# Kernel optimization log

Measured on AMD Instinct MI355X. Metric: run time of the kernel, lower is better.

Reference implementation:

```python
import jax, jax.numpy as jnp
import numpy as np

HEADS = 8
IN_CH = 768
INNER = 768
DK = INNER // HEADS


def setup_inputs() -> dict:
    key = jax.random.key(0)
    ks = jax.random.split(key, 9)
    bs, hw = 16, 1024
    s = 1.0 / np.sqrt(IN_CH)
    sp = 1.0 / np.sqrt(INNER)
    return {
        "x": jax.random.normal(ks[0], (bs, hw, IN_CH), jnp.float32),
        # weights stored (in, out) so y = x @ W + b (equiv to torch Linear)
        "Wq": jax.random.uniform(ks[1], (IN_CH, INNER), jnp.float32, -s, s),
        "bq": jax.random.uniform(ks[2], (INNER,), jnp.float32, -s, s),
        "Wk": jax.random.uniform(ks[3], (IN_CH, INNER), jnp.float32, -s, s),
        "bk": jax.random.uniform(ks[4], (INNER,), jnp.float32, -s, s),
        "Wv": jax.random.uniform(ks[5], (IN_CH, INNER), jnp.float32, -s, s),
        "bv": jax.random.uniform(ks[6], (INNER,), jnp.float32, -s, s),
        "Wp": jax.random.uniform(ks[7], (INNER, IN_CH), jnp.float32, -sp, sp),
        "bp": jax.random.uniform(ks[8], (IN_CH,), jnp.float32, -sp, sp),
    }


def reference(x, Wq, bq, Wk, bk, Wv, bv, Wp, bp):
    bs, hw, _ = x.shape
    # NOTE: the original torch code does .view(bs, heads, hw, dk) on a
    # (bs, hw, inner) tensor — a raw row-major reshape, not a head-split
    # transpose. Replicate exactly.
    q = (x @ Wq + bq).reshape(bs, HEADS, hw, DK)
    k = (x @ Wk + bk).reshape(bs, HEADS, hw, DK)
    v = (x @ Wv + bv).reshape(bs, HEADS, hw, DK)
    logits = jnp.einsum("bhqd,bhkd->bhqk", q, k) / np.sqrt(DK).astype(np.float32)
    attn = jax.nn.softmax(logits, axis=-1)
    out = jnp.einsum("bhqk,bhkd->bhqd", attn, v).reshape(bs, hw, INNER)
    # dropout is identity in eval mode
    return out @ Wp + bp
```

## Files before the change

kernel.cpp:

```cpp
#include <hip/hip_runtime.h>
#include <math.h>

typedef __bf16 bf16;
typedef __attribute__((ext_vector_type(8))) __bf16 bf16x8;
typedef __attribute__((ext_vector_type(4))) __bf16 bf16x4;
typedef __attribute__((ext_vector_type(4))) float f32x4;
typedef __attribute__((ext_vector_type(16))) float f32x16;

#define CE 0.14724445f
#define THR_RAW 54.0f

#define GLOAD16(g, l)                                                          \
    __builtin_amdgcn_global_load_lds(                                          \
        (const __attribute__((address_space(1))) void*)(g),                    \
        (__attribute__((address_space(3))) void*)(l), 16, 0, 0)

__global__ __launch_bounds__(256) void cvt_x(const float* __restrict__ x, bf16* __restrict__ xb) {
    size_t i = ((size_t)blockIdx.x * 256 + threadIdx.x) * 4;
    f32x4 v = *(const f32x4*)(x + i);
    bf16x4 o;
    o[0] = (bf16)v[0]; o[1] = (bf16)v[1]; o[2] = (bf16)v[2]; o[3] = (bf16)v[3];
    *(bf16x4*)(xb + i) = o;
}

struct WArgs { const float* w[4]; };

__global__ __launch_bounds__(256) void transpose_w(WArgs wa, bf16* __restrict__ out) {
    __shared__ float t[32][33];
    const int z = blockIdx.z;
    const float* __restrict__ W = wa.w[z];
    bf16* __restrict__ Wt = out + (size_t)z * 589824;
    int k0 = blockIdx.x * 32, n0 = blockIdx.y * 32;
    int tx = threadIdx.x, ty = threadIdx.y;
#pragma unroll
    for (int j = 0; j < 4; ++j)
        t[ty + j * 8][tx] = W[(size_t)(k0 + ty + j * 8) * 768 + n0 + tx];
    __syncthreads();
#pragma unroll
    for (int j = 0; j < 4; ++j)
        Wt[(size_t)(n0 + ty + j * 8) * 768 + k0 + tx] = (bf16)t[tx][ty + j * 8];
}

struct GemmArgs {
    const bf16* Bt[3];
    const float* bias[3];
    void* out[3];
};

template <bool F32OUT, int NZ>
__global__ __launch_bounds__(256, 2) void gemm_kernel(const bf16* __restrict__ A, GemmArgs ga) {
    __shared__ __align__(16) bf16 As[128 * 64];
    __shared__ __align__(16) bf16 Bs[128 * 64];
    const int nwg = gridDim.x;
    const int bid = blockIdx.x;
    const int lid = (bid & 7) * (nwg >> 3) + (bid >> 3);
    const int mt = lid / (6 * NZ);
    const int r0 = lid - mt * (6 * NZ);
    const int z  = r0 / 6;
    const int nt = r0 - z * 6;
    const int m0 = mt * 128;
    const int n0 = nt * 128;
    const bf16* __restrict__ Bt = ga.Bt[z];
    const int tid = threadIdx.x;
    const int lane = tid & 63, l15 = lane & 15, lq = lane >> 4;
    const int wid = tid >> 6;
    const int wm = (wid >> 1) * 64, wn = (wid & 1) * 64;

    const bf16* asrc[4]; const bf16* bsrc[4]; bf16* adst[4]; bf16* bdst[4];
#pragma unroll
    for (int i = 0; i < 4; ++i) {
        int r = (wid * 4 + i) * 8 + (lane >> 3);
        int s = lane & 7;
        int c = s ^ (r & 7);
        asrc[i] = A + (size_t)(m0 + r) * 768 + c * 8;
        bsrc[i] = Bt + (size_t)(n0 + r) * 768 + c * 8;
        adst[i] = As + (wid * 4 + i) * 512;
        bdst[i] = Bs + (wid * 4 + i) * 512;
    }

    f32x4 acc[4][4] = {};

    for (int ks = 0; ks < 768; ks += 64) {
#pragma unroll
        for (int i = 0; i < 4; ++i) {
            GLOAD16(asrc[i] + ks, adst[i]);
            GLOAD16(bsrc[i] + ks, bdst[i]);
        }
        __syncthreads();
#pragma unroll
        for (int kk = 0; kk < 2; ++kk) {
            bf16x8 af[4], bfr[4];
#pragma unroll
            for (int f = 0; f < 4; ++f) {
                int ar = wm + f * 16 + l15;
                int ac = (kk * 4 + lq) ^ (ar & 7);
                af[f] = *(const bf16x8*)(As + ar * 64 + ac * 8);
                int br = wn + f * 16 + l15;
                int bc = (kk * 4 + lq) ^ (br & 7);
                bfr[f] = *(const bf16x8*)(Bs + br * 64 + bc * 8);
            }
#pragma unroll
            for (int mf = 0; mf < 4; ++mf)
#pragma unroll
                for (int nf = 0; nf < 4; ++nf)
                    acc[mf][nf] = __builtin_amdgcn_mfma_f32_16x16x32_bf16(af[mf], bfr[nf], acc[mf][nf], 0, 0, 0);
        }
        __syncthreads();
    }
    const float* __restrict__ bias = ga.bias[z];
#pragma unroll
    for (int nf = 0; nf < 4; ++nf) {
        int col = n0 + wn + nf * 16 + l15;
        float bv = bias[col];
#pragma unroll
        for (int mf = 0; mf < 4; ++mf) {
            int rbase = m0 + wm + mf * 16 + lq * 4;
#pragma unroll
            for (int i = 0; i < 4; ++i) {
                float v = acc[mf][nf][i] + bv;
                if constexpr (F32OUT)
                    ((float*)ga.out[z])[(size_t)(rbase + i) * 768 + col] = v;
                else
                    ((bf16*)ga.out[z])[(size_t)(rbase + i) * 768 + col] = (bf16)v;
            }
        }
    }
}

__global__ __launch_bounds__(256) void transpose_v(const bf16* __restrict__ V, bf16* __restrict__ Vt) {
    __shared__ unsigned short t[64 * 97];
    const int g = blockIdx.y;
    const int kv0 = blockIdx.x * 64;
    const unsigned short* __restrict__ Vg = (const unsigned short*)V + (size_t)g * 98304;
    unsigned short* __restrict__ Vtg = (unsigned short*)Vt + (size_t)g * 98304;
    const int tid = threadIdx.x;
#pragma unroll
    for (int p = 0; p < 24; ++p) {
        int id = tid + p * 256;
        int row = id / 96, col = id % 96;
        t[row * 97 + col] = Vg[(size_t)(kv0 + row) * 96 + col];
    }
    __syncthreads();
#pragma unroll
    for (int p = 0; p < 24; ++p) {
        int id = tid + p * 256;
        int d = id >> 6, j = id & 63;
        Vtg[(size_t)d * 1024 + kv0 + j] = t[j * 97 + d];
    }
}

static __device__ inline int pk2(float a, float b) {
    union { __bf16 h[2]; int w; } u;
    u.h[0] = (__bf16)a; u.h[1] = (__bf16)b;
    return u.w;
}

static __device__ inline bf16x8 pack_step(float p0, float p1, float p2, float p3,
                                          float p4, float p5, float p6, float p7, int hi) {
    int A0 = pk2(p0, p1), A1 = pk2(p2, p3);
    int B0 = pk2(p4, p5), B1 = pk2(p6, p7);
    int t0 = hi ? A0 : B0;
    int t1 = hi ? A1 : B1;
    int x0 = __shfl_xor(t0, 32);
    int x1 = __shfl_xor(t1, 32);
    union { int w[4]; bf16x8 v; } u;
    u.w[0] = hi ? x0 : A0;
    u.w[1] = hi ? x1 : A1;
    u.w[2] = hi ? B0 : x0;
    u.w[3] = hi ? B1 : x1;
    return u.v;
}

__global__ __launch_bounds__(256, 3) void attn_kernel(const bf16* __restrict__ Q, const bf16* __restrict__ K,
                                                      const bf16* __restrict__ Vt, bf16* __restrict__ AO) {
    __shared__ __align__(16) bf16 Ks[12 * 64 * 8];
    __shared__ __align__(16) bf16 Vss[2 * 8 * 96 * 8];
    const int g = blockIdx.x;
    const int q0 = blockIdx.y * 128;
    const int tid = threadIdx.x;
    const int lane = tid & 63;
    const int l31 = lane & 31, hi = lane >> 5, wid = tid >> 6;
    const int qrow = q0 + wid * 32 + l31;
    const size_t gbase = (size_t)g * 98304;
    const bf16* __restrict__ Qg = Q + gbase;
    const bf16* __restrict__ Kg = K + gbase;
    const bf16* __restrict__ Vg = Vt + gbase;
    bf16* __restrict__ Og = AO + gbase;

    const bf16* ksrc[3]; bf16* kdst[3];
#pragma unroll
    for (int i = 0; i < 3; ++i) {
        int slot = wid * 3 + i;
        ksrc[i] = Kg + (size_t)lane * 96 + slot * 8;
        kdst[i] = Ks + slot * 512;
    }
    const bf16* vsrc[3]; int vdoff[3];
#pragma unroll
    for (int i = 0; i < 3; ++i) {
        int f = (wid * 3 + i) * 64 + lane;
        int slot = f / 96, row = f - slot * 96;
        vsrc[i] = Vg + (size_t)row * 1024 + slot * 8;
        vdoff[i] = (wid * 3 + i) * 512;
    }

    bf16x8 qf[6];
#pragma unroll
    for (int kk = 0; kk < 6; ++kk)
        qf[kk] = *(const bf16x8*)(Qg + (size_t)qrow * 96 + kk * 16 + hi * 8);

#pragma unroll
    for (int i = 0; i < 3; ++i) GLOAD16(ksrc[i], kdst[i]);
#pragma unroll
    for (int i = 0; i < 3; ++i) GLOAD16(vsrc[i], Vss + vdoff[i]);
    __syncthreads();
#pragma unroll
    for (int i = 0; i < 3; ++i) GLOAD16(vsrc[i] + 64, Vss + 6144 + vdoff[i]);

    f32x16 o[3] = {};
    float mrun = -INFINITY, lrun = 0.f;

    const bf16* kbase = Ks + hi * 512 + l31 * 8;

    for (int kt = 0; kt < 16; ++kt) {
        const bf16* vbase = Vss + (kt & 1) * 6144 + hi * 768 + l31 * 8;

        f32x16 s0 = {}, s1 = {};
        __builtin_amdgcn_s_setprio(1);
#pragma unroll
        for (int kk = 0; kk < 6; ++kk) {
            bf16x8 k0 = *(const bf16x8*)(kbase + kk * 1024);
            bf16x8 k1 = *(const bf16x8*)(kbase + kk * 1024 + 256);
            s0 = __builtin_amdgcn_mfma_f32_32x32x16_bf16(k0, qf[kk], s0, 0, 0, 0);
            s1 = __builtin_amdgcn_mfma_f32_32x32x16_bf16(k1, qf[kk], s1, 0, 0, 0);
        }
        __builtin_amdgcn_s_setprio(0);
        __syncthreads();
        if (kt < 15) {
#pragma unroll
            for (int i = 0; i < 3; ++i) GLOAD16(ksrc[i] + (kt + 1) * 6144, kdst[i]);
        }

        float t0 = fmaxf(fmaxf(s0[0], s0[1]), fmaxf(s0[2], s0[3]));
        float t1 = fmaxf(fmaxf(s0[4], s0[5]), fmaxf(s0[6], s0[7]));
        float t2 = fmaxf(fmaxf(s0[8], s0[9]), fmaxf(s0[10], s0[11]));
        float t3 = fmaxf(fmaxf(s0[12], s0[13]), fmaxf(s0[14], s0[15]));
        float u0 = fmaxf(fmaxf(s1[0], s1[1]), fmaxf(s1[2], s1[3]));
        float u1 = fmaxf(fmaxf(s1[4], s1[5]), fmaxf(s1[6], s1[7]));
        float u2 = fmaxf(fmaxf(s1[8], s1[9]), fmaxf(s1[10], s1[11]));
        float u3 = fmaxf(fmaxf(s1[12], s1[13]), fmaxf(s1[14], s1[15]));
        float pmax = fmaxf(fmaxf(fmaxf(t0, t1), fmaxf(t2, t3)),
                           fmaxf(fmaxf(u0, u1), fmaxf(u2, u3)));
        pmax = fmaxf(pmax, __shfl_xor(pmax, 32));
        if (!__all(pmax - mrun <= THR_RAW)) {
            float newm = fmaxf(mrun, pmax);
            float alpha = __builtin_amdgcn_exp2f(CE * (mrun - newm));
            mrun = newm;
            lrun *= alpha;
#pragma unroll
            for (int df = 0; df < 3; ++df)
#pragma unroll
                for (int r = 0; r < 16; ++r) o[df][r] *= alpha;
        }
        float lsa = 0.f, lsb = 0.f;
#pragma unroll
        for (int r = 0; r < 16; ++r) {
            float p = __builtin_amdgcn_exp2f(CE * (s0[r] - mrun));
            s0[r] = p; lsa += p;
        }
#pragma unroll
        for (int r = 0; r < 16; ++r) {
            float p = __builtin_amdgcn_exp2f(CE * (s1[r] - mrun));
            s1[r] = p; lsb += p;
        }
        float lsum = lsa + lsb;
        lsum += __shfl_xor(lsum, 32);
        lrun += lsum;

        bf16x8 pb0 = pack_step(s0[0], s0[1], s0[2], s0[3], s0[4], s0[5], s0[6], s0[7], hi);
        bf16x8 pb1 = pack_step(s0[8], s0[9], s0[10], s0[11], s0[12], s0[13], s0[14], s0[15], hi);
        bf16x8 pb2 = pack_step(s1[0], s1[1], s1[2], s1[3], s1[4], s1[5], s1[6], s1[7], hi);
        bf16x8 pb3 = pack_step(s1[8], s1[9], s1[10], s1[11], s1[12], s1[13], s1[14], s1[15], hi);
        __builtin_amdgcn_s_setprio(1);
#pragma unroll
        for (int df = 0; df < 3; ++df) {
            bf16x8 v0 = *(const bf16x8*)(vbase + 0 * 1536 + df * 256);
            bf16x8 v1 = *(const bf16x8*)(vbase + 1 * 1536 + df * 256);
            bf16x8 v2 = *(const bf16x8*)(vbase + 2 * 1536 + df * 256);
            bf16x8 v3 = *(const bf16x8*)(vbase + 3 * 1536 + df * 256);
            o[df] = __builtin_amdgcn_mfma_f32_32x32x16_bf16(v0, pb0, o[df], 0, 0, 0);
            o[df] = __builtin_amdgcn_mfma_f32_32x32x16_bf16(v1, pb1, o[df], 0, 0, 0);
            o[df] = __builtin_amdgcn_mfma_f32_32x32x16_bf16(v2, pb2, o[df], 0, 0, 0);
            o[df] = __builtin_amdgcn_mfma_f32_32x32x16_bf16(v3, pb3, o[df], 0, 0, 0);
        }
        __builtin_amdgcn_s_setprio(0);
        __syncthreads();
        if (kt < 14) {
#pragma unroll
            for (int i = 0; i < 3; ++i)
                GLOAD16(vsrc[i] + (kt + 2) * 64, Vss + (kt & 1) * 6144 + vdoff[i]);
        }
    }

    float inv = 1.0f / lrun;
#pragma unroll
    for (int df = 0; df < 3; ++df)
#pragma unroll
        for (int rq = 0; rq < 4; ++rq) {
            bf16x4 ov;
#pragma unroll
            for (int j = 0; j < 4; ++j) ov[j] = (bf16)(o[df][rq * 4 + j] * inv);
            *(bf16x4*)(Og + (size_t)qrow * 96 + df * 32 + rq * 8 + hi * 4) = ov;
        }
}

extern "C" void kernel_launch(void* const* d_in, const int* in_sizes, int n_in,
                              void* d_out, int out_size, void* d_ws, size_t ws_size,
                              hipStream_t stream) {
    const float* x  = (const float*)d_in[0];
    const float* Wq = (const float*)d_in[1];
    const float* bq = (const float*)d_in[2];
    const float* Wk = (const float*)d_in[3];
    const float* bk = (const float*)d_in[4];
    const float* Wv = (const float*)d_in[5];
    const float* bv = (const float*)d_in[6];
    const float* Wp = (const float*)d_in[7];
    const float* bp = (const float*)d_in[8];

    char* ws = (char*)d_ws;
    bf16* xb  = (bf16*)(ws);
    bf16* wt  = (bf16*)(ws + 25165824);
    bf16* Qb  = (bf16*)(ws + 29884416);
    bf16* Kb  = (bf16*)(ws + 55050240);
    bf16* Vb  = (bf16*)(ws + 80216064);
    bf16* Vtb = (bf16*)(ws + 105381888);
    bf16* AO  = xb;

    cvt_x<<<12288, 256, 0, stream>>>(x, xb);

    WArgs wa;
    wa.w[0] = Wq; wa.w[1] = Wk; wa.w[2] = Wv; wa.w[3] = Wp;
    transpose_w<<<dim3(24, 24, 4), dim3(32, 8), 0, stream>>>(wa, wt);

    GemmArgs g1{};
    g1.Bt[0] = wt;            g1.Bt[1] = wt + 589824;  g1.Bt[2] = wt + 2 * 589824;
    g1.bias[0] = bq;          g1.bias[1] = bk;         g1.bias[2] = bv;
    g1.out[0] = Qb;           g1.out[1] = Kb;          g1.out[2] = Vb;
    gemm_kernel<false, 3><<<2304, 256, 0, stream>>>(xb, g1);

    transpose_v<<<dim3(16, 128), 256, 0, stream>>>(Vb, Vtb);

    attn_kernel<<<dim3(128, 8), 256, 0, stream>>>(Qb, Kb, Vtb, AO);

    GemmArgs g2{};
    g2.Bt[0] = wt + 3 * 589824; g2.bias[0] = bp; g2.out[0] = (void*)d_out;
    g2.Bt[1] = g2.Bt[0]; g2.Bt[2] = g2.Bt[0];
    g2.bias[1] = bp; g2.bias[2] = bp;
    g2.out[1] = g2.out[0]; g2.out[2] = g2.out[0];
    gemm_kernel<true, 1><<<768, 256, 0, stream>>>(AO, g2);
}
```

Measured before the change: 199.4 us.

## Double attention block to 512 threads covering 256 queries per K/V tile

The attention kernel now runs 8 waves per block over 256 query rows instead of 4 waves over 128, so each K/V tile staged in LDS is reused by twice as many queries. This halves global K/V traffic and the number of blocks. The cooperative load distribution is reworked so each wave issues two guarded 16-byte loads, with waves 6 and 7 idle during loads. Launch bounds change to 512 threads with 4 blocks per CU, which may force the register budget down and cause spills. Every block-wide barrier now also synchronises twice as many waves.

```diff
diff --git a/kernel.cpp b/kernel.cpp
--- a/kernel.cpp
+++ b/kernel.cpp
@@ -171,12 +171,12 @@
     return u.v;
 }
 
-__global__ __launch_bounds__(256, 3) void attn_kernel(const bf16* __restrict__ Q, const bf16* __restrict__ K,
+__global__ __launch_bounds__(512, 4) void attn_kernel(const bf16* __restrict__ Q, const bf16* __restrict__ K,
                                                       const bf16* __restrict__ Vt, bf16* __restrict__ AO) {
     __shared__ __align__(16) bf16 Ks[12 * 64 * 8];
     __shared__ __align__(16) bf16 Vss[2 * 8 * 96 * 8];
     const int g = blockIdx.x;
-    const int q0 = blockIdx.y * 128;
+    const int q0 = blockIdx.y * 256;
     const int tid = threadIdx.x;
     const int lane = tid & 63;
     const int l31 = lane & 31, hi = lane >> 5, wid = tid >> 6;
@@ -187,20 +187,20 @@
     const bf16* __restrict__ Vg = Vt + gbase;
     bf16* __restrict__ Og = AO + gbase;
 
-    const bf16* ksrc[3]; bf16* kdst[3];
-#pragma unroll
-    for (int i = 0; i < 3; ++i) {
-        int slot = wid * 3 + i;
-        ksrc[i] = Kg + (size_t)lane * 96 + slot * 8;
-        kdst[i] = Ks + slot * 512;
-    }
-    const bf16* vsrc[3]; int vdoff[3];
-#pragma unroll
-    for (int i = 0; i < 3; ++i) {
-        int f = (wid * 3 + i) * 64 + lane;
-        int slot = f / 96, row = f - slot * 96;
-        vsrc[i] = Vg + (size_t)row * 1024 + slot * 8;
-        vdoff[i] = (wid * 3 + i) * 512;
+    const bf16* ksrc[2]; bf16* kdst[2]; bool kact[2];
+    const bf16* vsrc[2]; int vdoff[2]; bool vact[2];
+#pragma unroll
+    for (int i = 0; i < 2; ++i) {
+        int slot = wid * 2 + i;
+        kact[i] = slot < 12;
+        ksrc[i] = Kg + (size_t)lane * 96 + (kact[i] ? slot : 0) * 8;
+        kdst[i] = Ks + (kact[i] ? slot : 0) * 512;
+        int j = wid * 2 + i;
+        vact[i] = j < 12;
+        int f = (vact[i] ? j : 0) * 64 + lane;
+        int vs = f / 96, vr = f - vs * 96;
+        vsrc[i] = Vg + (size_t)vr * 1024 + vs * 8;
+        vdoff[i] = (vact[i] ? j : 0) * 512;
     }
 
     bf16x8 qf[6];
@@ -209,12 +209,12 @@
         qf[kk] = *(const bf16x8*)(Qg + (size_t)qrow * 96 + kk * 16 + hi * 8);
 
 #pragma unroll
-    for (int i = 0; i < 3; ++i) GLOAD16(ksrc[i], kdst[i]);
-#pragma unroll
-    for (int i = 0; i < 3; ++i) GLOAD16(vsrc[i], Vss + vdoff[i]);
+    for (int i = 0; i < 2; ++i) if (kact[i]) GLOAD16(ksrc[i], kdst[i]);
+#pragma unroll
+    for (int i = 0; i < 2; ++i) if (vact[i]) GLOAD16(vsrc[i], Vss + vdoff[i]);
     __syncthreads();
 #pragma unroll
-    for (int i = 0; i < 3; ++i) GLOAD16(vsrc[i] + 64, Vss + 6144 + vdoff[i]);
+    for (int i = 0; i < 2; ++i) if (vact[i]) GLOAD16(vsrc[i] + 64, Vss + 6144 + vdoff[i]);
 
     f32x16 o[3] = {};
     float mrun = -INFINITY, lrun = 0.f;
@@ -237,7 +237,7 @@
         __syncthreads();
         if (kt < 15) {
 #pragma unroll
-            for (int i = 0; i < 3; ++i) GLOAD16(ksrc[i] + (kt + 1) * 6144, kdst[i]);
+            for (int i = 0; i < 2; ++i) if (kact[i]) GLOAD16(ksrc[i] + (kt + 1) * 6144, kdst[i]);
         }
 
         float t0 = fmaxf(fmaxf(s0[0], s0[1]), fmaxf(s0[2], s0[3]));
@@ -296,8 +296,8 @@
         __syncthreads();
         if (kt < 14) {
 #pragma unroll
-            for (int i = 0; i < 3; ++i)
-                GLOAD16(vsrc[i] + (kt + 2) * 64, Vss + (kt & 1) * 6144 + vdoff[i]);
+            for (int i = 0; i < 2; ++i)
+                if (vact[i]) GLOAD16(vsrc[i] + (kt + 2) * 64, Vss + (kt & 1) * 6144 + vdoff[i]);
         }
     }
 
@@ -349,7 +349,7 @@
 
     transpose_v<<<dim3(16, 128), 256, 0, stream>>>(Vb, Vtb);
 
-    attn_kernel<<<dim3(128, 8), 256, 0, stream>>>(Qb, Kb, Vtb, AO);
+    attn_kernel<<<dim3(128, 4), 512, 0, stream>>>(Qb, Kb, Vtb, AO);
 
     GemmArgs g2{};
     g2.Bt[0] = wt + 3 * 589824; g2.bias[0] = bp; g2.out[0] = (void*)d_out;
```

New measurement: 203.2 us. No clear change (+1.9%).

## Double-buffer LDS tiles in GEMM and attention kernels to overlap loads

Applied to the files above, without the earlier changes.

The GEMM kernel gets two LDS buffers per operand, so the next K-tile is prefetched while MFMAs run on the current one. Its MFMA block is wrapped in setprio and its launch bound is raised to 3 waves. The attention kernel now double-buffers K and V together, prefetching both at the top of each iteration with one barrier per step instead of two. The cost is doubled LDS use in the GEMM (64KB per block), which may limit the targeted occupancy. Because the attention kernel drops the barrier after QK^T, correctness now depends on the single end-of-loop barrier protecting both buffers.

```diff
diff --git a/kernel.cpp b/kernel.cpp
--- a/kernel.cpp
+++ b/kernel.cpp
@@ -48,9 +48,9 @@
 };
 
 template <bool F32OUT, int NZ>
-__global__ __launch_bounds__(256, 2) void gemm_kernel(const bf16* __restrict__ A, GemmArgs ga) {
-    __shared__ __align__(16) bf16 As[128 * 64];
-    __shared__ __align__(16) bf16 Bs[128 * 64];
+__global__ __launch_bounds__(256, 3) void gemm_kernel(const bf16* __restrict__ A, GemmArgs ga) {
+    __shared__ __align__(16) bf16 As[2][8192];
+    __shared__ __align__(16) bf16 Bs[2][8192];
     const int nwg = gridDim.x;
     const int bid = blockIdx.x;
     const int lid = (bid & 7) * (nwg >> 3) + (bid >> 3);
@@ -66,7 +66,7 @@
     const int wid = tid >> 6;
     const int wm = (wid >> 1) * 64, wn = (wid & 1) * 64;
 
-    const bf16* asrc[4]; const bf16* bsrc[4]; bf16* adst[4]; bf16* bdst[4];
+    const bf16* asrc[4]; const bf16* bsrc[4]; int sdst[4];
 #pragma unroll
     for (int i = 0; i < 4; ++i) {
         int r = (wid * 4 + i) * 8 + (lane >> 3);
@@ -74,19 +74,28 @@
         int c = s ^ (r & 7);
         asrc[i] = A + (size_t)(m0 + r) * 768 + c * 8;
         bsrc[i] = Bt + (size_t)(n0 + r) * 768 + c * 8;
-        adst[i] = As + (wid * 4 + i) * 512;
-        bdst[i] = Bs + (wid * 4 + i) * 512;
+        sdst[i] = (wid * 4 + i) * 512;
     }
 
     f32x4 acc[4][4] = {};
 
-    for (int ks = 0; ks < 768; ks += 64) {
-#pragma unroll
-        for (int i = 0; i < 4; ++i) {
-            GLOAD16(asrc[i] + ks, adst[i]);
-            GLOAD16(bsrc[i] + ks, bdst[i]);
-        }
-        __syncthreads();
+#pragma unroll
+    for (int i = 0; i < 4; ++i) {
+        GLOAD16(asrc[i], &As[0][sdst[i]]);
+        GLOAD16(bsrc[i], &Bs[0][sdst[i]]);
+    }
+    __syncthreads();
+
+    for (int t = 0; t < 12; ++t) {
+        const int cur = t & 1, nxt = cur ^ 1;
+        if (t < 11) {
+            int ks = (t + 1) * 64;
+#pragma unroll
+            for (int i = 0; i < 4; ++i) {
+                GLOAD16(asrc[i] + ks, &As[nxt][sdst[i]]);
+                GLOAD16(bsrc[i] + ks, &Bs[nxt][sdst[i]]);
+            }
+        }
 #pragma unroll
         for (int kk = 0; kk < 2; ++kk) {
             bf16x8 af[4], bfr[4];
@@ -94,16 +103,18 @@
             for (int f = 0; f < 4; ++f) {
                 int ar = wm + f * 16 + l15;
                 int ac = (kk * 4 + lq) ^ (ar & 7);
-                af[f] = *(const bf16x8*)(As + ar * 64 + ac * 8);
+                af[f] = *(const bf16x8*)(&As[cur][ar * 64 + ac * 8]);
                 int br = wn + f * 16 + l15;
                 int bc = (kk * 4 + lq) ^ (br & 7);
-                bfr[f] = *(const bf16x8*)(Bs + br * 64 + bc * 8);
+                bfr[f] = *(const bf16x8*)(&Bs[cur][br * 64 + bc * 8]);
             }
+            __builtin_amdgcn_s_setprio(1);
 #pragma unroll
             for (int mf = 0; mf < 4; ++mf)
 #pragma unroll
                 for (int nf = 0; nf < 4; ++nf)
                     acc[mf][nf] = __builtin_amdgcn_mfma_f32_16x16x32_bf16(af[mf], bfr[nf], acc[mf][nf], 0, 0, 0);
+            __builtin_amdgcn_s_setprio(0);
         }
         __syncthreads();
     }
@@ -173,8 +184,8 @@
 
 __global__ __launch_bounds__(256, 3) void attn_kernel(const bf16* __restrict__ Q, const bf16* __restrict__ K,
                                                       const bf16* __restrict__ Vt, bf16* __restrict__ AO) {
-    __shared__ __align__(16) bf16 Ks[12 * 64 * 8];
-    __shared__ __align__(16) bf16 Vss[2 * 8 * 96 * 8];
+    __shared__ __align__(16) bf16 Ks[2][12 * 512];
+    __shared__ __align__(16) bf16 Vs[2][12 * 512];
     const int g = blockIdx.x;
     const int q0 = blockIdx.y * 128;
     const int tid = threadIdx.x;
@@ -187,20 +198,17 @@
     const bf16* __restrict__ Vg = Vt + gbase;
     bf16* __restrict__ Og = AO + gbase;
 
-    const bf16* ksrc[3]; bf16* kdst[3];
+    const bf16* ksrc[3]; int kdo[3];
+    const bf16* vsrc[3]; int vdo[3];
 #pragma unroll
     for (int i = 0; i < 3; ++i) {
         int slot = wid * 3 + i;
         ksrc[i] = Kg + (size_t)lane * 96 + slot * 8;
-        kdst[i] = Ks + slot * 512;
-    }
-    const bf16* vsrc[3]; int vdoff[3];
-#pragma unroll
-    for (int i = 0; i < 3; ++i) {
+        kdo[i] = slot * 512;
         int f = (wid * 3 + i) * 64 + lane;
-        int slot = f / 96, row = f - slot * 96;
-        vsrc[i] = Vg + (size_t)row * 1024 + slot * 8;
-        vdoff[i] = (wid * 3 + i) * 512;
+        int vs = f / 96, vr = f - vs * 96;
+        vsrc[i] = Vg + (size_t)vr * 1024 + vs * 8;
+        vdo[i] = (wid * 3 + i) * 512;
     }
 
     bf16x8 qf[6];
@@ -209,20 +217,26 @@
         qf[kk] = *(const bf16x8*)(Qg + (size_t)qrow * 96 + kk * 16 + hi * 8);
 
 #pragma unroll
-    for (int i = 0; i < 3; ++i) GLOAD16(ksrc[i], kdst[i]);
-#pragma unroll
-    for (int i = 0; i < 3; ++i) GLOAD16(vsrc[i], Vss + vdoff[i]);
+    for (int i = 0; i < 3; ++i) {
+        GLOAD16(ksrc[i], &Ks[0][kdo[i]]);
+        GLOAD16(vsrc[i], &Vs[0][vdo[i]]);
+    }
     __syncthreads();
-#pragma unroll
-    for (int i = 0; i < 3; ++i) GLOAD16(vsrc[i] + 64, Vss + 6144 + vdoff[i]);
 
     f32x16 o[3] = {};
     float mrun = -INFINITY, lrun = 0.f;
 
-    const bf16* kbase = Ks + hi * 512 + l31 * 8;
-
     for (int kt = 0; kt < 16; ++kt) {
-        const bf16* vbase = Vss + (kt & 1) * 6144 + hi * 768 + l31 * 8;
+        const int cur = kt & 1, nxt = cur ^ 1;
+        if (kt < 15) {
+#pragma unroll
+            for (int i = 0; i < 3; ++i) {
+                GLOAD16(ksrc[i] + (kt + 1) * 6144, &Ks[nxt][kdo[i]]);
+                GLOAD16(vsrc[i] + (kt + 1) * 64, &Vs[nxt][vdo[i]]);
+            }
+        }
+        const bf16* kbase = &Ks[cur][hi * 512 + l31 * 8];
+        const bf16* vbase = &Vs[cur][hi * 768 + l31 * 8];
 
         f32x16 s0 = {}, s1 = {};
         __builtin_amdgcn_s_setprio(1);
@@ -234,11 +248,6 @@
             s1 = __builtin_amdgcn_mfma_f32_32x32x16_bf16(k1, qf[kk], s1, 0, 0, 0);
         }
         __builtin_amdgcn_s_setprio(0);
-        __syncthreads();
-        if (kt < 15) {
-#pragma unroll
-            for (int i = 0; i < 3; ++i) GLOAD16(ksrc[i] + (kt + 1) * 6144, kdst[i]);
-        }
 
         float t0 = fmaxf(fmaxf(s0[0], s0[1]), fmaxf(s0[2], s0[3]));
         float t1 = fmaxf(fmaxf(s0[4], s0[5]), fmaxf(s0[6], s0[7]));
@@ -294,11 +303,6 @@
         }
         __builtin_amdgcn_s_setprio(0);
         __syncthreads();
-        if (kt < 14) {
-#pragma unroll
-            for (int i = 0; i < 3; ++i)
-                GLOAD16(vsrc[i] + (kt + 2) * 64, Vss + (kt & 1) * 6144 + vdoff[i]);
-        }
     }
 
     float inv = 1.0f / lrun;
```

After: 227.4 us. 1.14x slower.

## Fuse fp32-to-bf16 conversion of x into QKV GEMM and vectorize V transpose

Applied to the files above, without the earlier changes.

Removes the separate cvt_x kernel and has the QKV GEMM read fp32 x directly. It converts x to bf16 in registers before storing to swizzled LDS, prefetching the next k-slab into registers during the MFMA loop. The change is meant to eliminate a full bf16 write and read of x plus one launch. The cost is that A-tile global reads are twice as wide and repeated across many workgroups, and that the async LDS-load path is replaced for A. The V transpose also switches to 4-element vector loads and stores to cut instruction count.

```diff
diff --git a/kernel.cpp b/kernel.cpp
--- a/kernel.cpp
+++ b/kernel.cpp
@@ -6,6 +6,7 @@
 typedef __attribute__((ext_vector_type(4))) __bf16 bf16x4;
 typedef __attribute__((ext_vector_type(4))) float f32x4;
 typedef __attribute__((ext_vector_type(16))) float f32x16;
+typedef __attribute__((ext_vector_type(4))) unsigned short u16x4;
 
 #define CE 0.14724445f
 #define THR_RAW 54.0f
@@ -14,14 +15,6 @@
     __builtin_amdgcn_global_load_lds(                                          \
         (const __attribute__((address_space(1))) void*)(g),                    \
         (__attribute__((address_space(3))) void*)(l), 16, 0, 0)
-
-__global__ __launch_bounds__(256) void cvt_x(const float* __restrict__ x, bf16* __restrict__ xb) {
-    size_t i = ((size_t)blockIdx.x * 256 + threadIdx.x) * 4;
-    f32x4 v = *(const f32x4*)(x + i);
-    bf16x4 o;
-    o[0] = (bf16)v[0]; o[1] = (bf16)v[1]; o[2] = (bf16)v[2]; o[3] = (bf16)v[3];
-    *(bf16x4*)(xb + i) = o;
-}
 
 struct WArgs { const float* w[4]; };
 
@@ -47,8 +40,8 @@
     void* out[3];
 };
 
-template <bool F32OUT, int NZ>
-__global__ __launch_bounds__(256, 2) void gemm_kernel(const bf16* __restrict__ A, GemmArgs ga) {
+template <bool F32OUT, int NZ, bool AF32>
+__global__ __launch_bounds__(256, 2) void gemm_kernel(const void* __restrict__ Av, GemmArgs ga) {
     __shared__ __align__(16) bf16 As[128 * 64];
     __shared__ __align__(16) bf16 Bs[128 * 64];
     const int nwg = gridDim.x;
@@ -66,35 +59,76 @@
     const int wid = tid >> 6;
     const int wm = (wid >> 1) * 64, wn = (wid & 1) * 64;
 
-    const bf16* asrc[4]; const bf16* bsrc[4]; bf16* adst[4]; bf16* bdst[4];
+    const bf16* bsrc[4]; bf16* bdst[4];
 #pragma unroll
     for (int i = 0; i < 4; ++i) {
         int r = (wid * 4 + i) * 8 + (lane >> 3);
         int s = lane & 7;
         int c = s ^ (r & 7);
-        asrc[i] = A + (size_t)(m0 + r) * 768 + c * 8;
         bsrc[i] = Bt + (size_t)(n0 + r) * 768 + c * 8;
-        adst[i] = As + (wid * 4 + i) * 512;
         bdst[i] = Bs + (wid * 4 + i) * 512;
     }
 
+    const bf16* agsrc[4]; bf16* agdst[4];
+    const float* afsrc = nullptr;
+    int awoff[4];
+    const int ra = tid >> 1;
+    const int ha = (tid & 1) * 4;
+    if constexpr (AF32) {
+        afsrc = (const float*)Av + (size_t)(m0 + ra) * 768 + ha * 8;
+#pragma unroll
+        for (int j = 0; j < 4; ++j)
+            awoff[j] = ra * 64 + ((ha + j) ^ (ra & 7)) * 8;
+    } else {
+#pragma unroll
+        for (int i = 0; i < 4; ++i) {
+            int r = (wid * 4 + i) * 8 + (lane >> 3);
+            int s = lane & 7;
+            int c = s ^ (r & 7);
+            agsrc[i] = (const bf16*)Av + (size_t)(m0 + r) * 768 + c * 8;
+            agdst[i] = As + (wid * 4 + i) * 512;
+        }
+    }
+
     f32x4 acc[4][4] = {};
-
-    for (int ks = 0; ks < 768; ks += 64) {
-#pragma unroll
-        for (int i = 0; i < 4; ++i) {
-            GLOAD16(asrc[i] + ks, adst[i]);
-            GLOAD16(bsrc[i] + ks, bdst[i]);
-        }
+    f32x4 ar[8];
+
+    if constexpr (AF32) {
+#pragma unroll
+        for (int j = 0; j < 8; ++j) ar[j] = *(const f32x4*)(afsrc + j * 4);
+    }
+
+    for (int t = 0; t < 12; ++t) {
+        const int ks = t * 64;
+        if constexpr (AF32) {
+#pragma unroll
+            for (int j = 0; j < 4; ++j) {
+                bf16x8 ch;
+#pragma unroll
+                for (int e = 0; e < 4; ++e) { ch[e] = (bf16)ar[2 * j][e]; ch[e + 4] = (bf16)ar[2 * j + 1][e]; }
+                *(bf16x8*)(As + awoff[j]) = ch;
+            }
+        } else {
+#pragma unroll
+            for (int i = 0; i < 4; ++i) GLOAD16(agsrc[i] + ks, agdst[i]);
+        }
+#pragma unroll
+        for (int i = 0; i < 4; ++i) GLOAD16(bsrc[i] + ks, bdst[i]);
         __syncthreads();
+        if constexpr (AF32) {
+            if (t < 11) {
+#pragma unroll
+                for (int j = 0; j < 8; ++j) ar[j] = *(const f32x4*)(afsrc + (ks + 64) + j * 4);
+            }
+        }
 #pragma unroll
         for (int kk = 0; kk < 2; ++kk) {
             bf16x8 af[4], bfr[4];
 #pragma unroll
             for (int f = 0; f < 4; ++f) {
-                int ar = wm + f * 16 + l15;
-                int ac = (kk * 4 + lq) ^ (ar & 7);
-                af[f] = *(const bf16x8*)(As + ar * 64 + ac * 8);
+                int arow = wm + f * 16 + l15;
+                int ac = (kk * 4 + lq) ^ (arow & 7);
+                af[f] = *(const bf16x8*)(As + arow * 64 + ac * 8);
                 int br = wn + f * 16 + l15;
                 int bc = (kk * 4 + lq) ^ (br & 7);
                 bfr[f] = *(const bf16x8*)(Bs + br * 64 + bc * 8);
@@ -135,17 +169,22 @@
     unsigned short* __restrict__ Vtg = (unsigned short*)Vt + (size_t)g * 98304;
     const int tid = threadIdx.x;
 #pragma unroll
-    for (int p = 0; p < 24; ++p) {
+    for (int p = 0; p < 6; ++p) {
         int id = tid + p * 256;
-        int row = id / 96, col = id % 96;
-        t[row * 97 + col] = Vg[(size_t)(kv0 + row) * 96 + col];
+        int row = id / 24, c4 = id % 24;
+        u16x4 v = *(const u16x4*)(Vg + (size_t)(kv0 + row) * 96 + c4 * 4);
+#pragma unroll
+        for (int k = 0; k < 4; ++k) t[row * 97 + c4 * 4 + k] = v[k];
     }
     __syncthreads();
 #pragma unroll
-    for (int p = 0; p < 24; ++p) {
+    for (int p = 0; p < 6; ++p) {
         int id = tid + p * 256;
-        int d = id >> 6, j = id & 63;
-        Vtg[(size_t)d * 1024 + kv0 + j] = t[j * 97 + d];
+        int d = id / 16, j4 = id % 16;
+        u16x4 v;
+#pragma unroll
+        for (int k = 0; k < 4; ++k) v[k] = t[(j4 * 4 + k) * 97 + d];
+        *(u16x4*)(Vtg + (size_t)d * 1024 + kv0 + j4 * 4) = v;
     }
 }
 
@@ -327,15 +366,12 @@
     const float* bp = (const float*)d_in[8];
 
     char* ws = (char*)d_ws;
-    bf16* xb  = (bf16*)(ws);
-    bf16* wt  = (bf16*)(ws + 25165824);
-    bf16* Qb  = (bf16*)(ws + 29884416);
-    bf16* Kb  = (bf16*)(ws + 55050240);
-    bf16* Vb  = (bf16*)(ws + 80216064);
-    bf16* Vtb = (bf16*)(ws + 105381888);
-    bf16* AO  = xb;
-
-    cvt_x<<<12288, 256, 0, stream>>>(x, xb);
+    bf16* wt  = (bf16*)(ws);
+    bf16* Qb  = (bf16*)(ws + 4718592);
+    bf16* Kb  = (bf16*)(ws + 29884416);
+    bf16* Vb  = (bf16*)(ws + 55050240);
+    bf16* Vtb = (bf16*)(ws + 80216064);
+    bf16* AO  = (bf16*)(ws + 105381888);
 
     WArgs wa;
     wa.w[0] = Wq; wa.w[1] = Wk; wa.w[2] = Wv; wa.w[3] = Wp;
@@ -345,7 +381,7 @@
     g1.Bt[0] = wt;            g1.Bt[1] = wt + 589824;  g1.Bt[2] = wt + 2 * 589824;
     g1.bias[0] = bq;          g1.bias[1] = bk;         g1.bias[2] = bv;
     g1.out[0] = Qb;           g1.out[1] = Kb;          g1.out[2] = Vb;
-    gemm_kernel<false, 3><<<2304, 256, 0, stream>>>(xb, g1);
+    gemm_kernel<false, 3, true><<<2304, 256, 0, stream>>>((const void*)x, g1);
 
     transpose_v<<<dim3(16, 128), 256, 0, stream>>>(Vb, Vtb);
 
@@ -356,5 +392,5 @@
     g2.Bt[1] = g2.Bt[0]; g2.Bt[2] = g2.Bt[0];
     g2.bias[1] = bp; g2.bias[2] = bp;
     g2.out[1] = g2.out[0]; g2.out[2] = g2.out[0];
-    gemm_kernel<true, 1><<<768, 256, 0, stream>>>(AO, g2);
-}
+    gemm_kernel<true, 1, false><<<768, 256, 0, stream>>>((const void*)AO, g2);
+}
```

New measurement: 266.5 us. 1.34x slower.
